# Optimization experiments

Hardware: AMD Instinct MI355X
Metric: run time of the kernel (lower is better)

## Reference

```python
import jax, jax.numpy as jnp
import numpy as np

EMBED_DIM = 1024
NUM_HEADS = 16
HEAD_DIM = EMBED_DIM // NUM_HEADS


def setup_inputs() -> dict:
    key = jax.random.key(0)
    ks = jax.random.split(key, 5)
    x = jax.random.normal(ks[0], (2, 2048, EMBED_DIM), dtype=jnp.float32)
    s_in = 1.0 / np.sqrt(EMBED_DIM)
    W_qkv = jax.random.uniform(ks[1], (EMBED_DIM, 3 * EMBED_DIM), minval=-s_in, maxval=s_in, dtype=jnp.float32)
    b_qkv = jax.random.uniform(ks[2], (3 * EMBED_DIM,), minval=-s_in, maxval=s_in, dtype=jnp.float32)
    W_out = jax.random.uniform(ks[3], (EMBED_DIM, EMBED_DIM), minval=-s_in, maxval=s_in, dtype=jnp.float32)
    b_out = jax.random.uniform(ks[4], (EMBED_DIM,), minval=-s_in, maxval=s_in, dtype=jnp.float32)
    return {"x": x, "W_qkv": W_qkv, "b_qkv": b_qkv, "W_out": W_out, "b_out": b_out}


def reference(x, W_qkv, b_qkv, W_out, b_out):
    B, S, D = x.shape
    H, Dh = NUM_HEADS, HEAD_DIM
    qkv = x @ W_qkv + b_qkv                       # [B, S, 3D]
    q, k, v = jnp.split(qkv, 3, axis=-1)
    # [B, S, D] -> [B, H, S, Dh]
    q = q.reshape(B, S, H, Dh).transpose(0, 2, 1, 3)
    k = k.reshape(B, S, H, Dh).transpose(0, 2, 1, 3)
    v = v.reshape(B, S, H, Dh).transpose(0, 2, 1, 3)
    scores = jnp.einsum('bhqd,bhkd->bhqk', q, k) / jnp.sqrt(jnp.float32(Dh))
    probs = jax.nn.softmax(scores, axis=-1)       # [B, H, S, S]
    attn = jnp.einsum('bhqk,bhkd->bhqd', probs, v)
    attn = attn.transpose(0, 2, 1, 3).reshape(B, S, D)
    return attn @ W_out + b_out
```

## Files before the change

### kernel.cpp

```cpp
#include <hip/hip_runtime.h>
#include <hip/hip_bf16.h>

#define DEV __device__ __forceinline__

typedef __bf16 bf16x8 __attribute__((ext_vector_type(8)));
typedef float f32x4 __attribute__((ext_vector_type(4)));
typedef float f32x16 __attribute__((ext_vector_type(16)));
using u16 = unsigned short;
using u32 = unsigned int;

static constexpr int S = 2048;
static constexpr int D = 1024;
static constexpr float SCQ = 0.125f * 1.44269504088896340736f;

DEV u16 f2bf(float f) {
  unsigned u = __builtin_bit_cast(unsigned, f);
  u += 0x7fffu + ((u >> 16) & 1u);
  return (u16)(u >> 16);
}
DEV u16 f2bfr(float f) {
  return (u16)((__builtin_bit_cast(u32, f) + 0x8000u) >> 16);
}
DEV u32 pk2(float a, float b) {
  u32 ua = __builtin_bit_cast(u32, a) + 0x8000u;
  u32 ub = __builtin_bit_cast(u32, b) + 0x8000u;
  return __builtin_amdgcn_perm(ub, ua, 0x07060302);
}

DEV void gl16(const u16* __restrict__ g, u16* l) {
  __builtin_amdgcn_global_load_lds((const __attribute__((address_space(1))) u32*)g,
                                   (__attribute__((address_space(3))) u32*)l, 16, 0, 0);
}

__global__ __launch_bounds__(256) void k_prep(const float* __restrict__ x, u16* __restrict__ Xb,
                                              const float* __restrict__ Wqkv, u16* __restrict__ WqkvT,
                                              const float* __restrict__ Wout, u16* __restrict__ WoutT) {
  __shared__ float t[32][33];
  const int bid = blockIdx.x;
  const int tid = threadIdx.x;
  if (bid < 4096) {
    const int i = bid * 256 + tid;
    const float4 v = reinterpret_cast<const float4*>(x)[i];
    ushort4 o;
    o.x = f2bf(v.x); o.y = f2bf(v.y); o.z = f2bf(v.z); o.w = f2bf(v.w);
    reinterpret_cast<ushort4*>(Xb)[i] = o;
    return;
  }
  const float* in;
  u16* out;
  int R, C, bx, by;
  if (bid < 4096 + 3072) {
    const int b = bid - 4096;
    in = Wqkv; out = WqkvT; R = 1024; C = 3072;
    bx = b % 96; by = b / 96;
  } else {
    const int b = bid - 7168;
    in = Wout; out = WoutT; R = 1024; C = 1024;
    bx = b & 31; by = b >> 5;
  }
  const int tx = tid & 31, ty = tid >> 5;
  const int c0 = bx * 32, r0 = by * 32;
  for (int i = ty; i < 32; i += 8)
    t[i][tx] = in[(size_t)(r0 + i) * C + c0 + tx];
  __syncthreads();
  for (int i = ty; i < 32; i += 8)
    out[(size_t)(c0 + i) * R + r0 + tx] = f2bf(t[tx][i]);
}

__global__ __launch_bounds__(256, 3) void k_gemm0(const u16* __restrict__ A, const u16* __restrict__ Bt,
                                                  const float* __restrict__ bias, int M, int N, int K,
                                                  u16* __restrict__ Qb, u16* __restrict__ Kb,
                                                  u16* __restrict__ Vt) {
  constexpr int TN = 128, NJ = 4;
  constexpr int BSZ = 128 * 32 * 2;
  __shared__ __align__(16) char smem[3 * 2 * BSZ];
  auto As = reinterpret_cast<u16(*)[128][32]>(smem);
  auto Bs = reinterpret_cast<u16(*)[128][32]>(smem + 3 * BSZ);
  auto LT = reinterpret_cast<u16(*)[136]>(smem);
  const int tid = threadIdx.x;
  const int lane = tid & 63, wave = tid >> 6;
  const int l15 = lane & 15, quad = lane >> 4;
  const int bid0 = blockIdx.x + 24 * blockIdx.y;
  const int bid = (bid0 & 7) * 96 + (bid0 >> 3);
  const int m0 = (bid / 24) * 128, n0 = (bid % 24) * TN;
  const int wm = (wave >> 1) * 64, wn = (wave & 1) * (TN / 2);
  const int lr = lane >> 2;
  const int lcs = ((((lane & 3) - (lane >> 3)) & 3)) * 8;
  const int sq = ((quad + (l15 >> 1)) & 3) * 8;

  f32x4 acc[4][NJ];
#pragma unroll
  for (int i = 0; i < 4; i++)
#pragma unroll
    for (int j = 0; j < NJ; j++) acc[i][j] = (f32x4){0.f, 0.f, 0.f, 0.f};

  const u16* Aw0 = &A[(size_t)(m0 + wave * 32 + lr) * K + lcs];
  const u16* Aw1 = &A[(size_t)(m0 + wave * 32 + 16 + lr) * K + lcs];
  const u16* Bw0 = &Bt[(size_t)(n0 + wave * 32 + lr) * K + lcs];
  const u16* Bw1 = &Bt[(size_t)(n0 + wave * 32 + 16 + lr) * K + lcs];

  gl16(Aw0, &As[0][wave * 32][0]);
  gl16(Aw1, &As[0][wave * 32 + 16][0]);
  gl16(Bw0, &Bs[0][wave * 32][0]);
  gl16(Bw1, &Bs[0][wave * 32 + 16][0]);
  gl16(Aw0 + 32, &As[1][wave * 32][0]);
  gl16(Aw1 + 32, &As[1][wave * 32 + 16][0]);
  gl16(Bw0 + 32, &Bs[1][wave * 32][0]);
  gl16(Bw1 + 32, &Bs[1][wave * 32 + 16][0]);

  int cur = 0, nx2 = 2;
  for (int kk = 0; kk < K; kk += 32) {
    if (kk + 32 < K) asm volatile("s_waitcnt vmcnt(4)" ::: "memory");
    else             asm volatile("s_waitcnt vmcnt(0)" ::: "memory");
    __builtin_amdgcn_s_barrier();
    __builtin_amdgcn_sched_barrier(0);
    if (kk + 64 < K) {
      gl16(Aw0 + kk + 64, &As[nx2][wave * 32][0]);
      gl16(Aw1 + kk + 64, &As[nx2][wave * 32 + 16][0]);
      gl16(Bw0 + kk + 64, &Bs[nx2][wave * 32][0]);
      gl16(Bw1 + kk + 64, &Bs[nx2][wave * 32 + 16][0]);
    }
    bf16x8 af[4], bfv[NJ];
#pragma unroll
    for (int i = 0; i < 4; i++)
      af[i] = *reinterpret_cast<const bf16x8*>(&As[cur][wm + i * 16 + l15][sq]);
#pragma unroll
    for (int j = 0; j < NJ; j++)
      bfv[j] = *reinterpret_cast<const bf16x8*>(&Bs[cur][wn + j * 16 + l15][sq]);
#pragma unroll
    for (int i = 0; i < 4; i++)
#pragma unroll
      for (int j = 0; j < NJ; j++)
        acc[i][j] = __builtin_amdgcn_mfma_f32_16x16x32_bf16(af[i], bfv[j], acc[i][j], 0, 0, 0);
    cur = (cur == 2) ? 0 : cur + 1;
    nx2 = (nx2 == 2) ? 0 : nx2 + 1;
  }

  if (n0 >= 2048) {
    const int b = m0 >> 11, sbase = m0 & 2047;
#pragma unroll
    for (int p = 0; p < 2; p++) {
      __syncthreads();
      if ((wave & 1) == p) {
#pragma unroll
        for (int j = 0; j < NJ; j++) {
          const int n = n0 + wn + j * 16 + l15;
          const float vb = bias[n];
#pragma unroll
          for (int i = 0; i < 4; i++) {
            uint2 pw;
            pw.x = pk2(acc[i][j][0] + vb, acc[i][j][1] + vb);
            pw.y = pk2(acc[i][j][2] + vb, acc[i][j][3] + vb);
            *reinterpret_cast<uint2*>(&LT[j * 16 + l15][wm + i * 16 + quad * 4]) = pw;
          }
        }
      }
      __syncthreads();
      const int h = ((n0 - 2048) >> 6) + p;
      const int bh = b * 16 + h;
      const int nl = tid >> 2, cc = (tid & 3) * 32;
      u16* dst = &Vt[((size_t)bh * 64 + nl) * S + sbase + cc];
#pragma unroll
      for (int k = 0; k < 4; k++)
        reinterpret_cast<uint4*>(dst)[k] = *reinterpret_cast<const uint4*>(&LT[nl][cc + k * 8]);
    }
  } else {
#pragma unroll
    for (int i = 0; i < 4; i++) {
#pragma unroll
      for (int j = 0; j < NJ; j++) {
#pragma unroll
        for (int r = 0; r < 4; r++) {
          const int m = m0 + wm + i * 16 + quad * 4 + r;
          const int n = n0 + wn + j * 16 + l15;
          const float v = acc[i][j][r] + bias[n];
          const int h = (n >> 6) & 15, dh = n & 63;
          const int b = m >> 11, s = m & 2047;
          const int bh = b * 16 + h;
          if (n < 1024) Qb[((size_t)bh * S + s) * 64 + dh] = f2bfr(v * SCQ);
          else          Kb[((size_t)bh * S + s) * 64 + dh] = f2bfr(v);
        }
      }
    }
  }
}

__global__ __launch_bounds__(256, 2) void k_gemm2(const u16* __restrict__ A, const u16* __restrict__ Bt,
                                                  const float* __restrict__ bias, float* __restrict__ outF) {
  constexpr int K = 1024, N = 1024;
  constexpr int ABSZ = 128 * 64 * 2;
  constexpr int BBSZ = 64 * 64 * 2;
  __shared__ __align__(16) char smem[3 * (ABSZ + BBSZ)];
  auto As = reinterpret_cast<u16(*)[128][64]>(smem);
  auto Bs = reinterpret_cast<u16(*)[64][64]>(smem + 3 * ABSZ);
  const int tid = threadIdx.x;
  const int lane = tid & 63, wave = tid >> 6;
  const int l15 = lane & 15, quad = lane >> 4;
  const int bid0 = blockIdx.x + 16 * blockIdx.y;
  const int bid = (bid0 & 7) * 64 + (bid0 >> 3);
  const int m0 = (bid >> 4) * 128, n0 = (bid & 15) * 64;
  const int wm = (wave >> 1) * 64, wn = (wave & 1) * 32;
  const int srow = lane >> 3;
  const int scol = ((lane & 7) ^ srow) * 8;

  f32x4 acc[4][2];
#pragma unroll
  for (int i = 0; i < 4; i++)
#pragma unroll
    for (int j = 0; j < 2; j++) acc[i][j] = (f32x4){0.f, 0.f, 0.f, 0.f};

  const u16* Ap[4];
  const u16* Bp[2];
#pragma unroll
  for (int c = 0; c < 4; c++)
    Ap[c] = &A[(size_t)(m0 + (wave * 4 + c) * 8 + srow) * K + scol];
#pragma unroll
  for (int c = 0; c < 2; c++)
    Bp[c] = &Bt[(size_t)(n0 + (wave * 2 + c) * 8 + srow) * K + scol];

#pragma unroll
  for (int c = 0; c < 4; c++) gl16(Ap[c], &As[0][(wave * 4 + c) * 8][0]);
#pragma unroll
  for (int c = 0; c < 2; c++) gl16(Bp[c], &Bs[0][(wave * 2 + c) * 8][0]);
#pragma unroll
  for (int c = 0; c < 4; c++) gl16(Ap[c] + 64, &As[1][(wave * 4 + c) * 8][0]);
#pragma unroll
  for (int c = 0; c < 2; c++) gl16(Bp[c] + 64, &Bs[1][(wave * 2 + c) * 8][0]);

  int cur = 0, nx2 = 2;
  for (int kk = 0; kk < K; kk += 64) {
    if (kk + 64 < K) asm volatile("s_waitcnt vmcnt(6)" ::: "memory");
    else             asm volatile("s_waitcnt vmcnt(0)" ::: "memory");
    __builtin_amdgcn_s_barrier();
    __builtin_amdgcn_sched_barrier(0);
    if (kk + 128 < K) {
#pragma unroll
      for (int c = 0; c < 4; c++) gl16(Ap[c] + kk + 128, &As[nx2][(wave * 4 + c) * 8][0]);
#pragma unroll
      for (int c = 0; c < 2; c++) gl16(Bp[c] + kk + 128, &Bs[nx2][(wave * 2 + c) * 8][0]);
    }
#pragma unroll
    for (int ks = 0; ks < 2; ks++) {
      const int sc = ((ks * 4 + quad) ^ (l15 & 7)) * 8;
      bf16x8 af[4], bfv[2];
#pragma unroll
      for (int i = 0; i < 4; i++)
        af[i] = *reinterpret_cast<const bf16x8*>(&As[cur][wm + i * 16 + l15][sc]);
#pragma unroll
      for (int j = 0; j < 2; j++)
        bfv[j] = *reinterpret_cast<const bf16x8*>(&Bs[cur][wn + j * 16 + l15][sc]);
#pragma unroll
      for (int i = 0; i < 4; i++)
#pragma unroll
        for (int j = 0; j < 2; j++)
          acc[i][j] = __builtin_amdgcn_mfma_f32_16x16x32_bf16(af[i], bfv[j], acc[i][j], 0, 0, 0);
    }
    cur = (cur == 2) ? 0 : cur + 1;
    nx2 = (nx2 == 2) ? 0 : nx2 + 1;
  }

#pragma unroll
  for (int i = 0; i < 4; i++)
#pragma unroll
    for (int j = 0; j < 2; j++)
#pragma unroll
      for (int r = 0; r < 4; r++) {
        const int m = m0 + wm + i * 16 + quad * 4 + r;
        const int n = n0 + wn + j * 16 + l15;
        outF[(size_t)m * N + n] = acc[i][j][r] + bias[n];
      }
}

__global__ __launch_bounds__(256, 2) void k_attn(const u16* __restrict__ Qb,
                                                 const u16* __restrict__ Kb,
                                                 const u16* __restrict__ Vt,
                                                 u16* __restrict__ attnB) {
  __shared__ u16 Ks[2][64][72];
  __shared__ u16 Vs[2][64][72];
  __shared__ u16 Pl[4][32][72];
  const int tid = threadIdx.x;
  const int lane = tid & 63, wave = tid >> 6;
  const int l31 = lane & 31, hi = lane >> 5;
  const int bid0 = blockIdx.x + 16 * blockIdx.y;
  const int bid = (bid0 & 7) * 64 + (bid0 >> 3);
  const int bh = bid >> 4;
  const int q0 = (bid & 15) * 128;
  const u16* Qh = Qb + (size_t)bh * S * 64;
  const u16* Kh = Kb + (size_t)bh * S * 64;
  const u16* Vh = Vt + (size_t)bh * 64 * S;
  const int qrow = q0 + wave * 32 + l31;
  bf16x8 qf[4];
#pragma unroll
  for (int f = 0; f < 4; f++)
    qf[f] = *reinterpret_cast<const bf16x8*>(&Qh[(size_t)qrow * 64 + f * 16 + hi * 8]);

  const int r0 = tid >> 3, c0 = (tid & 7) * 8;

  float li = 0.f;
  f32x16 o0, o1;
#pragma unroll
  for (int r = 0; r < 16; r++) { o0[r] = 0.f; o1[r] = 0.f; }

  uint4 pk0 = *reinterpret_cast<const uint4*>(&Kh[(size_t)r0 * 64 + c0]);
  uint4 pk1 = *reinterpret_cast<const uint4*>(&Kh[(size_t)(r0 + 32) * 64 + c0]);
  uint4 pv0 = *reinterpret_cast<const uint4*>(&Vh[(size_t)r0 * S + c0]);
  uint4 pv1 = *reinterpret_cast<const uint4*>(&Vh[(size_t)(r0 + 32) * S + c0]);
  *reinterpret_cast<uint4*>(&Ks[0][r0][c0]) = pk0;
  *reinterpret_cast<uint4*>(&Ks[0][r0 + 32][c0]) = pk1;
  *reinterpret_cast<uint4*>(&Vs[0][r0][c0]) = pv0;
  *reinterpret_cast<uint4*>(&Vs[0][r0 + 32][c0]) = pv1;
  {
    const u16* Kn = Kh + (size_t)64 * 64;
    pk0 = *reinterpret_cast<const uint4*>(&Kn[(size_t)r0 * 64 + c0]);
    pk1 = *reinterpret_cast<const uint4*>(&Kn[(size_t)(r0 + 32) * 64 + c0]);
    pv0 = *reinterpret_cast<const uint4*>(&Vh[(size_t)r0 * S + 64 + c0]);
    pv1 = *reinterpret_cast<const uint4*>(&Vh[(size_t)(r0 + 32) * S + 64 + c0]);
  }

  constexpr int NT = S / 64;
  for (int kb = 0; kb < NT; kb++) {
    const int cur = kb & 1, nxt = cur ^ 1;
    __syncthreads();
    if (kb + 1 < NT) {
      *reinterpret_cast<uint4*>(&Ks[nxt][r0][c0]) = pk0;
      *reinterpret_cast<uint4*>(&Ks[nxt][r0 + 32][c0]) = pk1;
      *reinterpret_cast<uint4*>(&Vs[nxt][r0][c0]) = pv0;
      *reinterpret_cast<uint4*>(&Vs[nxt][r0 + 32][c0]) = pv1;
    }
    if (kb + 2 < NT) {
      const u16* Kn = Kh + (size_t)(kb + 2) * 64 * 64;
      pk0 = *reinterpret_cast<const uint4*>(&Kn[(size_t)r0 * 64 + c0]);
      pk1 = *reinterpret_cast<const uint4*>(&Kn[(size_t)(r0 + 32) * 64 + c0]);
      pv0 = *reinterpret_cast<const uint4*>(&Vh[(size_t)r0 * S + (kb + 2) * 64 + c0]);
      pv1 = *reinterpret_cast<const uint4*>(&Vh[(size_t)(r0 + 32) * S + (kb + 2) * 64 + c0]);
    }
    f32x16 z[2];
    __builtin_amdgcn_s_setprio(1);
#pragma unroll
    for (int kt = 0; kt < 2; kt++) {
#pragma unroll
      for (int r = 0; r < 16; r++) z[kt][r] = 0.f;
#pragma unroll
      for (int f = 0; f < 4; f++) {
        const bf16x8 a = *reinterpret_cast<const bf16x8*>(&Ks[cur][kt * 32 + l31][f * 16 + hi * 8]);
        z[kt] = __builtin_amdgcn_mfma_f32_32x32x16_bf16(a, qf[f], z[kt], 0, 0, 0);
      }
    }
    __builtin_amdgcn_s_setprio(0);
    float s0 = 0.f, s1 = 0.f, s2 = 0.f, s3 = 0.f;
#pragma unroll
    for (int kt = 0; kt < 2; kt++)
#pragma unroll
      for (int r = 0; r < 16; r++) {
        const float p = __builtin_amdgcn_exp2f(z[kt][r]);
        z[kt][r] = p;
        if ((r & 3) == 0) s0 += p; else if ((r & 3) == 1) s1 += p;
        else if ((r & 3) == 2) s2 += p; else s3 += p;
      }
    li += (s0 + s1) + (s2 + s3);
    __builtin_amdgcn_s_setprio(1);
#pragma unroll
    for (int kt = 0; kt < 2; kt++) {
#pragma unroll
      for (int s = 0; s < 2; s++) {
        u32 w0 = pk2(z[kt][s * 8 + 0], z[kt][s * 8 + 1]);
        u32 w2 = pk2(z[kt][s * 8 + 4], z[kt][s * 8 + 5]);
        asm("v_permlane32_swap_b32 %0, %1" : "+v"(w0), "+v"(w2));
        u32 w1 = pk2(z[kt][s * 8 + 2], z[kt][s * 8 + 3]);
        u32 w3 = pk2(z[kt][s * 8 + 6], z[kt][s * 8 + 7]);
        asm("v_permlane32_swap_b32 %0, %1" : "+v"(w1), "+v"(w3));
        uint4 wv;
        wv.x = w0; wv.y = w1; wv.z = w2; wv.w = w3;
        const bf16x8 bp = __builtin_bit_cast(bf16x8, wv);
        const int f = kt * 2 + s;
        const bf16x8 av0 = *reinterpret_cast<const bf16x8*>(&Vs[cur][l31][f * 16 + hi * 8]);
        const bf16x8 av1 = *reinterpret_cast<const bf16x8*>(&Vs[cur][32 + l31][f * 16 + hi * 8]);
        o0 = __builtin_amdgcn_mfma_f32_32x32x16_bf16(av0, bp, o0, 0, 0, 0);
        o1 = __builtin_amdgcn_mfma_f32_32x32x16_bf16(av1, bp, o1, 0, 0, 0);
      }
    }
    __builtin_amdgcn_s_setprio(0);
  }
  li += __shfl_xor(li, 32);
  const float inv = 1.f / li;
#pragma unroll
  for (int dt = 0; dt < 2; dt++) {
    const f32x16& od = dt ? o1 : o0;
#pragma unroll
    for (int g = 0; g < 4; g++) {
      uint2 ow;
      ow.x = pk2(od[g * 4 + 0] * inv, od[g * 4 + 1] * inv);
      ow.y = pk2(od[g * 4 + 2] * inv, od[g * 4 + 3] * inv);
      *reinterpret_cast<uint2*>(&Pl[wave][l31][dt * 32 + g * 8 + hi * 4]) = ow;
    }
  }
  const int b = bh >> 4, h = bh & 15;
  const int mbase = b * S + q0 + wave * 32;
  const int qr = lane >> 1, ch = (lane & 1) * 32;
  u16* dst = &attnB[(size_t)(mbase + qr) * D + h * 64 + ch];
#pragma unroll
  for (int c = 0; c < 4; c++)
    reinterpret_cast<uint4*>(dst)[c] = *reinterpret_cast<const uint4*>(&Pl[wave][qr][ch + c * 8]);
}

extern "C" void kernel_launch(void* const* d_in, const int* in_sizes, int n_in,
                              void* d_out, int out_size, void* d_ws, size_t ws_size,
                              hipStream_t stream) {
  const float* x = (const float*)d_in[0];
  const float* Wqkv = (const float*)d_in[1];
  const float* bqkv = (const float*)d_in[2];
  const float* Wout = (const float*)d_in[3];
  const float* bout = (const float*)d_in[4];
  float* out = (float*)d_out;

  char* p = (char*)d_ws;
  u16* WoutT = (u16*)p; p += (size_t)1024 * 1024 * 2;
  u16* attnB = (u16*)p; p += (size_t)4096 * 1024 * 2;
  u16* Xb = (u16*)p;    p += (size_t)4096 * 1024 * 2;
  u16* WqkvT = (u16*)p; p += (size_t)3072 * 1024 * 2;
  u16* Vt = (u16*)p;    p += (size_t)32 * 64 * 2048 * 2;
  u16* Qb = (u16*)p;    p += (size_t)32 * 2048 * 64 * 2;
  u16* Kb = (u16*)p;    p += (size_t)32 * 2048 * 64 * 2;

  k_prep<<<4096 + 3072 + 1024, 256, 0, stream>>>(x, Xb, Wqkv, WqkvT, Wout, WoutT);
  k_gemm0<<<dim3(3072 / 128, 4096 / 128), 256, 0, stream>>>(
      Xb, WqkvT, bqkv, 4096, 3072, 1024, Qb, Kb, Vt);
  k_attn<<<dim3(2048 / 128, 32), 256, 0, stream>>>(Qb, Kb, Vt, attnB);
  k_gemm2<<<dim3(1024 / 64, 4096 / 128), 256, 0, stream>>>(attnB, WoutT, bout, out);
}
```

Before: 174.7 us.

## Software-pipeline attention loop so QK of one tile overlaps softmax/PV of previous

Restructures the attention inner loop into a two-stage software pipeline. The QK^T MFMAs for key block kb are issued alongside the exp/pack/PV MFMAs for block kb-1, using ping-pong score registers. V shared memory goes to triple buffering so the previous block's V stays valid, and the global prefetch distance drops from two tiles to one. The aim is to hide softmax VALU latency behind matrix work, at the cost of more live VGPRs and less slack on global load latency.

```diff
diff --git a/kernel.cpp b/kernel.cpp
--- a/kernel.cpp
+++ b/kernel.cpp
@@ -271,12 +271,68 @@
       }
 }
 
+DEV void qk_produce(f32x16& z0, f32x16& z1, const u16 (*Ksb)[72],
+                    const bf16x8* qf, int l31, int hi) {
+#pragma unroll
+  for (int r = 0; r < 16; r++) { z0[r] = 0.f; z1[r] = 0.f; }
+  __builtin_amdgcn_s_setprio(1);
+#pragma unroll
+  for (int f = 0; f < 4; f++) {
+    const bf16x8 a0 = *reinterpret_cast<const bf16x8*>(&Ksb[l31][f * 16 + hi * 8]);
+    const bf16x8 a1 = *reinterpret_cast<const bf16x8*>(&Ksb[32 + l31][f * 16 + hi * 8]);
+    z0 = __builtin_amdgcn_mfma_f32_32x32x16_bf16(a0, qf[f], z0, 0, 0, 0);
+    z1 = __builtin_amdgcn_mfma_f32_32x32x16_bf16(a1, qf[f], z1, 0, 0, 0);
+  }
+  __builtin_amdgcn_s_setprio(0);
+}
+
+DEV void pv_half(const f32x16& z, int f0, const u16 (*Vsb)[72], int l31, int hi,
+                 f32x16& o0, f32x16& o1) {
+#pragma unroll
+  for (int s = 0; s < 2; s++) {
+    u32 w0 = pk2(z[s * 8 + 0], z[s * 8 + 1]);
+    u32 w2 = pk2(z[s * 8 + 4], z[s * 8 + 5]);
+    asm("v_permlane32_swap_b32 %0, %1" : "+v"(w0), "+v"(w2));
+    u32 w1 = pk2(z[s * 8 + 2], z[s * 8 + 3]);
+    u32 w3 = pk2(z[s * 8 + 6], z[s * 8 + 7]);
+    asm("v_permlane32_swap_b32 %0, %1" : "+v"(w1), "+v"(w3));
+    uint4 wv;
+    wv.x = w0; wv.y = w1; wv.z = w2; wv.w = w3;
+    const bf16x8 bp = __builtin_bit_cast(bf16x8, wv);
+    const int f = f0 + s;
+    const bf16x8 av0 = *reinterpret_cast<const bf16x8*>(&Vsb[l31][f * 16 + hi * 8]);
+    const bf16x8 av1 = *reinterpret_cast<const bf16x8*>(&Vsb[32 + l31][f * 16 + hi * 8]);
+    o0 = __builtin_amdgcn_mfma_f32_32x32x16_bf16(av0, bp, o0, 0, 0, 0);
+    o1 = __builtin_amdgcn_mfma_f32_32x32x16_bf16(av1, bp, o1, 0, 0, 0);
+  }
+}
+
+DEV void sm_pv(f32x16& z0, f32x16& z1, const u16 (*Vsb)[72], int l31, int hi,
+               float& li, f32x16& o0, f32x16& o1) {
+  float s0 = 0.f, s1 = 0.f, s2 = 0.f, s3 = 0.f;
+#pragma unroll
+  for (int r = 0; r < 16; r++) {
+    const float p0 = __builtin_amdgcn_exp2f(z0[r]);
+    const float p1 = __builtin_amdgcn_exp2f(z1[r]);
+    z0[r] = p0; z1[r] = p1;
+    if ((r & 3) == 0) { s0 += p0; s0 += p1; }
+    else if ((r & 3) == 1) { s1 += p0; s1 += p1; }
+    else if ((r & 3) == 2) { s2 += p0; s2 += p1; }
+    else { s3 += p0; s3 += p1; }
+  }
+  li += (s0 + s1) + (s2 + s3);
+  __builtin_amdgcn_s_setprio(1);
+  pv_half(z0, 0, Vsb, l31, hi, o0, o1);
+  pv_half(z1, 2, Vsb, l31, hi, o0, o1);
+  __builtin_amdgcn_s_setprio(0);
+}
+
 __global__ __launch_bounds__(256, 2) void k_attn(const u16* __restrict__ Qb,
                                                  const u16* __restrict__ Kb,
                                                  const u16* __restrict__ Vt,
                                                  u16* __restrict__ attnB) {
   __shared__ u16 Ks[2][64][72];
-  __shared__ u16 Vs[2][64][72];
+  __shared__ u16 Vs[3][64][72];
   __shared__ u16 Pl[4][32][72];
   const int tid = threadIdx.x;
   const int lane = tid & 63, wave = tid >> 6;
@@ -300,87 +356,42 @@
   f32x16 o0, o1;
 #pragma unroll
   for (int r = 0; r < 16; r++) { o0[r] = 0.f; o1[r] = 0.f; }
+  f32x16 zE0, zE1, zO0, zO1;
 
   uint4 pk0 = *reinterpret_cast<const uint4*>(&Kh[(size_t)r0 * 64 + c0]);
   uint4 pk1 = *reinterpret_cast<const uint4*>(&Kh[(size_t)(r0 + 32) * 64 + c0]);
   uint4 pv0 = *reinterpret_cast<const uint4*>(&Vh[(size_t)r0 * S + c0]);
   uint4 pv1 = *reinterpret_cast<const uint4*>(&Vh[(size_t)(r0 + 32) * S + c0]);
-  *reinterpret_cast<uint4*>(&Ks[0][r0][c0]) = pk0;
-  *reinterpret_cast<uint4*>(&Ks[0][r0 + 32][c0]) = pk1;
-  *reinterpret_cast<uint4*>(&Vs[0][r0][c0]) = pv0;
-  *reinterpret_cast<uint4*>(&Vs[0][r0 + 32][c0]) = pv1;
-  {
-    const u16* Kn = Kh + (size_t)64 * 64;
-    pk0 = *reinterpret_cast<const uint4*>(&Kn[(size_t)r0 * 64 + c0]);
-    pk1 = *reinterpret_cast<const uint4*>(&Kn[(size_t)(r0 + 32) * 64 + c0]);
-    pv0 = *reinterpret_cast<const uint4*>(&Vh[(size_t)r0 * S + 64 + c0]);
-    pv1 = *reinterpret_cast<const uint4*>(&Vh[(size_t)(r0 + 32) * S + 64 + c0]);
-  }
 
   constexpr int NT = S / 64;
-  for (int kb = 0; kb < NT; kb++) {
-    const int cur = kb & 1, nxt = cur ^ 1;
-    __syncthreads();
-    if (kb + 1 < NT) {
-      *reinterpret_cast<uint4*>(&Ks[nxt][r0][c0]) = pk0;
-      *reinterpret_cast<uint4*>(&Ks[nxt][r0 + 32][c0]) = pk1;
-      *reinterpret_cast<uint4*>(&Vs[nxt][r0][c0]) = pv0;
-      *reinterpret_cast<uint4*>(&Vs[nxt][r0 + 32][c0]) = pv1;
-    }
-    if (kb + 2 < NT) {
-      const u16* Kn = Kh + (size_t)(kb + 2) * 64 * 64;
-      pk0 = *reinterpret_cast<const uint4*>(&Kn[(size_t)r0 * 64 + c0]);
-      pk1 = *reinterpret_cast<const uint4*>(&Kn[(size_t)(r0 + 32) * 64 + c0]);
-      pv0 = *reinterpret_cast<const uint4*>(&Vh[(size_t)r0 * S + (kb + 2) * 64 + c0]);
-      pv1 = *reinterpret_cast<const uint4*>(&Vh[(size_t)(r0 + 32) * S + (kb + 2) * 64 + c0]);
-    }
-    f32x16 z[2];
-    __builtin_amdgcn_s_setprio(1);
-#pragma unroll
-    for (int kt = 0; kt < 2; kt++) {
-#pragma unroll
-      for (int r = 0; r < 16; r++) z[kt][r] = 0.f;
-#pragma unroll
-      for (int f = 0; f < 4; f++) {
-        const bf16x8 a = *reinterpret_cast<const bf16x8*>(&Ks[cur][kt * 32 + l31][f * 16 + hi * 8]);
-        z[kt] = __builtin_amdgcn_mfma_f32_32x32x16_bf16(a, qf[f], z[kt], 0, 0, 0);
-      }
-    }
-    __builtin_amdgcn_s_setprio(0);
-    float s0 = 0.f, s1 = 0.f, s2 = 0.f, s3 = 0.f;
-#pragma unroll
-    for (int kt = 0; kt < 2; kt++)
-#pragma unroll
-      for (int r = 0; r < 16; r++) {
-        const float p = __builtin_amdgcn_exp2f(z[kt][r]);
-        z[kt][r] = p;
-        if ((r & 3) == 0) s0 += p; else if ((r & 3) == 1) s1 += p;
-        else if ((r & 3) == 2) s2 += p; else s3 += p;
-      }
-    li += (s0 + s1) + (s2 + s3);
-    __builtin_amdgcn_s_setprio(1);
-#pragma unroll
-    for (int kt = 0; kt < 2; kt++) {
-#pragma unroll
-      for (int s = 0; s < 2; s++) {
-        u32 w0 = pk2(z[kt][s * 8 + 0], z[kt][s * 8 + 1]);
-        u32 w2 = pk2(z[kt][s * 8 + 4], z[kt][s * 8 + 5]);
-        asm("v_permlane32_swap_b32 %0, %1" : "+v"(w0), "+v"(w2));
-        u32 w1 = pk2(z[kt][s * 8 + 2], z[kt][s * 8 + 3]);
-        u32 w3 = pk2(z[kt][s * 8 + 6], z[kt][s * 8 + 7]);
-        asm("v_permlane32_swap_b32 %0, %1" : "+v"(w1), "+v"(w3));
-        uint4 wv;
-        wv.x = w0; wv.y = w1; wv.z = w2; wv.w = w3;
-        const bf16x8 bp = __builtin_bit_cast(bf16x8, wv);
-        const int f = kt * 2 + s;
-        const bf16x8 av0 = *reinterpret_cast<const bf16x8*>(&Vs[cur][l31][f * 16 + hi * 8]);
-        const bf16x8 av1 = *reinterpret_cast<const bf16x8*>(&Vs[cur][32 + l31][f * 16 + hi * 8]);
-        o0 = __builtin_amdgcn_mfma_f32_32x32x16_bf16(av0, bp, o0, 0, 0, 0);
-        o1 = __builtin_amdgcn_mfma_f32_32x32x16_bf16(av1, bp, o1, 0, 0, 0);
-      }
-    }
-    __builtin_amdgcn_s_setprio(0);
-  }
+
+#define ATTN_STEP(KB, ZC0, ZC1, ZP0, ZP1, DO_CONS)                                \
+  {                                                                               \
+    const int cur_ = (KB) & 1, vb_ = (KB) % 3;                                    \
+    *reinterpret_cast<uint4*>(&Ks[cur_][r0][c0]) = pk0;                           \
+    *reinterpret_cast<uint4*>(&Ks[cur_][r0 + 32][c0]) = pk1;                      \
+    *reinterpret_cast<uint4*>(&Vs[vb_][r0][c0]) = pv0;                            \
+    *reinterpret_cast<uint4*>(&Vs[vb_][r0 + 32][c0]) = pv1;                       \
+    if ((KB) + 1 < NT) {                                                          \
+      const u16* Kn_ = Kh + (size_t)((KB) + 1) * 64 * 64;                         \
+      const u16* Vn_ = Vh + (size_t)((KB) + 1) * 64;                              \
+      pk0 = *reinterpret_cast<const uint4*>(&Kn_[(size_t)r0 * 64 + c0]);          \
+      pk1 = *reinterpret_cast<const uint4*>(&Kn_[(size_t)(r0 + 32) * 64 + c0]);   \
+      pv0 = *reinterpret_cast<const uint4*>(&Vn_[(size_t)r0 * S + c0]);           \
+      pv1 = *reinterpret_cast<const uint4*>(&Vn_[(size_t)(r0 + 32) * S + c0]);    \
+    }                                                                             \
+    __syncthreads();                                                              \
+    qk_produce(ZC0, ZC1, Ks[cur_], qf, l31, hi);                                  \
+    if (DO_CONS) sm_pv(ZP0, ZP1, Vs[((KB) + 2) % 3], l31, hi, li, o0, o1);        \
+  }
+
+  for (int p = 0; p < NT / 2; p++) {
+    ATTN_STEP(2 * p,     zE0, zE1, zO0, zO1, p > 0);
+    ATTN_STEP(2 * p + 1, zO0, zO1, zE0, zE1, true);
+  }
+  sm_pv(zO0, zO1, Vs[(NT - 1) % 3], l31, hi, li, o0, o1);
+#undef ATTN_STEP
+
   li += __shfl_xor(li, 32);
   const float inv = 1.f / li;
 #pragma unroll
```

New measurement: 172.8 us, median of 3. Within noise of the previous version (-1.0%).
